# Kernel optimization log

Measured on AMD Instinct MI355X. Metric: run time of the kernel, lower is better.

The kernel has to match this reference:

```python
import jax, jax.numpy as jnp
import numpy as np
import math

B, L, H, E = 4, 2048, 16, 64
S, D = L, E


def setup_inputs() -> dict:
    key = jax.random.key(0)
    kq, kk, kv = jax.random.split(key, 3)
    queries = jax.random.normal(kq, (B, L, H, E), dtype=jnp.float32)
    keys = jax.random.normal(kk, (B, S, H, E), dtype=jnp.float32)
    values = jax.random.normal(kv, (B, S, H, D), dtype=jnp.float32)
    # TriangularCausalMask: True above the diagonal => masked out
    attn_mask = jnp.broadcast_to(
        jnp.triu(jnp.ones((L, S), dtype=bool), k=1)[None, None], (B, 1, L, S)
    )
    return {"queries": queries, "keys": keys, "values": values, "attn_mask": attn_mask}


def reference(queries, keys, values, attn_mask):
    Edim = queries.shape[-1]
    scale = 1.0 / math.sqrt(Edim)  # self.scale is None -> 1/sqrt(E)
    # scores: [B, H, L, S]
    scores = jnp.einsum("blhe,bshe->bhls", queries, keys)
    # mask BEFORE scaling (as in original); -inf is invariant under positive scale
    scores = jnp.where(attn_mask, -jnp.inf, scores)
    attn = jax.nn.softmax(scale * scores, axis=-1)  # dropout p=0.0 -> identity
    out = jnp.einsum("bhls,bshd->blhd", attn, values)
    return out
```

## Files before the change

kernel.cpp:

```cpp
#include <hip/hip_runtime.h>


#define B_ 4
#define L_ 2048
#define H_ 16

typedef __attribute__((ext_vector_type(4))) float f32x4;
typedef __attribute__((ext_vector_type(8))) short bf16x8;

#if __has_builtin(__builtin_amdgcn_exp2f)
#define EXP2(x) __builtin_amdgcn_exp2f(x)
#else
#define EXP2(x) exp2f(x)
#endif

#if __has_builtin(__builtin_amdgcn_sched_barrier)
#define SCHED_FENCE() __builtin_amdgcn_sched_barrier(0)
#else
#define SCHED_FENCE()
#endif

#define BAR() do {                                              \
    SCHED_FENCE();                                              \
    asm volatile("s_waitcnt lgkmcnt(0)" ::: "memory");          \
    __builtin_amdgcn_s_barrier();                               \
    SCHED_FENCE();                                              \
} while (0)

__device__ __forceinline__ unsigned pkbf(float lo, float hi) {
    union { float f; unsigned u; } a, b;
    a.f = lo; b.f = hi;
    return __builtin_amdgcn_perm(b.u, a.u, 0x07060302u);
}

__global__ __launch_bounds__(512, 2) void attn_fwd(
    const float* __restrict__ Q, const float* __restrict__ K,
    const float* __restrict__ V, float* __restrict__ O)
{
    __shared__ unsigned smem[9216];

    const int tid = threadIdx.x;
    const int w   = tid >> 6;
    const int l   = tid & 63;
    const int l15 = l & 15;
    const int qd  = l >> 4;
    const int bh  = blockIdx.x & 63;
    const int g   = blockIdx.x >> 6;
    const int u   = (g < 4) ? g : 11 - g;
    const int b   = bh >> 4, h = bh & 15;
    const float cexp = 0.125f * 1.44269504088896340736f;

    const float* Kb = K + (((size_t)b * L_) * H_ + h) * 64;
    const float* Vb = V + (((size_t)b * L_) * H_ + h) * 64;

    const int t    = 2 * u + (w >> 2);
    const int qr0  = t * 128 + (w & 3) * 32;
    const int mykb = (qr0 >> 6) + 1;
    const int nkb  = 4 * u + 4;

    const int krow = tid >> 3, kq = tid & 7;
    const int kmrow = (((krow >> 2) & 1) << 5) | (((krow >> 5) & 1) << 4)
                    | (((krow >> 3) & 3) << 2) | (krow & 3);
    const int vsp = tid >> 4;
    const int vdg = (tid >> 1) & 7;
    const int vh  = tid & 1;
    const int vswz = vsp ^ (4 * vdg);

    bf16x8 qf[2][2];
#pragma unroll
    for (int rt = 0; rt < 2; ++rt) {
        const int row = qr0 + 16 * rt + l15;
        const float* qp = Q + (((size_t)b * L_ + row) * H_ + h) * 64 + qd * 8;
#pragma unroll
        for (int ke = 0; ke < 2; ++ke) {
            float4 f0 = *(const float4*)(qp + ke * 32);
            float4 f1 = *(const float4*)(qp + ke * 32 + 4);
            union { unsigned u[4]; bf16x8 v; } cv;
            cv.u[0] = pkbf(f0.x * cexp, f0.y * cexp);
            cv.u[1] = pkbf(f0.z * cexp, f0.w * cexp);
            cv.u[2] = pkbf(f1.x * cexp, f1.y * cexp);
            cv.u[3] = pkbf(f1.z * cexp, f1.w * cexp);
            qf[rt][ke] = cv.v;
        }
    }

    f32x4 o[4][2];
#pragma unroll
    for (int dt = 0; dt < 4; ++dt)
#pragma unroll
        for (int rt = 0; rt < 2; ++rt)
            o[dt][rt] = (f32x4){0.f, 0.f, 0.f, 0.f};
    float ls[2] = {0.f, 0.f};

    {
        const float* kg = Kb + (size_t)krow * 1024 + kq * 8;
        float4 k0 = *(const float4*)(kg + 0);
        float4 k1 = *(const float4*)(kg + 4);
        const float* vg = Vb + (size_t)(2 * vsp) * 1024 + vdg * 8 + vh * 4;
        float4 v0 = *(const float4*)(vg + 0);
        float4 v1 = *(const float4*)(vg + 1024);
        unsigned* kd = smem + kmrow * 36 + kq * 4;
        uint4 w0;
        w0.x = pkbf(k0.x, k0.y); w0.y = pkbf(k0.z, k0.w);
        w0.z = pkbf(k1.x, k1.y); w0.w = pkbf(k1.z, k1.w);
        *(uint4*)kd = w0;
        unsigned* vd = smem + 2304 + (8 * vdg + 4 * vh) * 36 + vswz;
        vd[0 * 36] = pkbf(v0.x, v1.x);
        vd[1 * 36] = pkbf(v0.y, v1.y);
        vd[2 * 36] = pkbf(v0.z, v1.z);
        vd[3 * 36] = pkbf(v0.w, v1.w);
    }
    BAR();

    for (int kb = 0; kb < nkb; ++kb) {
        const bool more = (kb + 1 < nkb);
        float4 nk0, nk1, nv0, nv1;
        if (more) {
            const float* kg = Kb + (size_t)((kb + 1) * 64 + krow) * 1024 + kq * 8;
            nk0 = *(const float4*)(kg + 0);
            nk1 = *(const float4*)(kg + 4);
            const float* vg = Vb + (size_t)((kb + 1) * 64 + 2 * vsp) * 1024 + vdg * 8 + vh * 4;
            nv0 = *(const float4*)(vg + 0);
            nv1 = *(const float4*)(vg + 1024);
        }

        if (kb < mykb) {
            const unsigned* Kl = smem + (kb & 1) * 4608;
            const unsigned* Vl = Kl + 2304;

            f32x4 st[4][2];
#pragma unroll
            for (int kt = 0; kt < 4; ++kt)
#pragma unroll
                for (int rt = 0; rt < 2; ++rt)
                    st[kt][rt] = (f32x4){0.f, 0.f, 0.f, 0.f};
#pragma unroll
            for (int kt = 0; kt < 4; ++kt)
#pragma unroll
                for (int ke = 0; ke < 2; ++ke) {
                    bf16x8 a = *(const bf16x8*)(Kl + (kt * 16 + l15) * 36 + ke * 16 + qd * 4);
                    st[kt][0] = __builtin_amdgcn_mfma_f32_16x16x32_bf16(a, qf[0][ke], st[kt][0], 0, 0, 0);
                    st[kt][1] = __builtin_amdgcn_mfma_f32_16x16x32_bf16(a, qf[1][ke], st[kt][1], 0, 0, 0);
                }

            if (kb == mykb - 1) {
#pragma unroll
                for (int kt = 0; kt < 4; ++kt)
#pragma unroll
                    for (int rt = 0; rt < 2; ++rt) {
                        const int rowg = qr0 + 16 * rt + l15;
#pragma unroll
                        for (int r = 0; r < 4; ++r) {
                            const int key = kb * 64 + (kt & 1) * 32 + qd * 8
                                          + (kt >> 1) * 4 + r;
                            if (key > rowg) st[kt][rt][r] = -1e30f;
                        }
                    }
            }

            float sacc0 = 0.f, sacc1 = 0.f;
#pragma unroll
            for (int kt = 0; kt < 4; ++kt)
#pragma unroll
                for (int r = 0; r < 4; ++r) {
                    float p0 = EXP2(st[kt][0][r]);
                    float p1 = EXP2(st[kt][1][r]);
                    st[kt][0][r] = p0;
                    st[kt][1][r] = p1;
                    sacc0 += p0;
                    sacc1 += p1;
                }
            ls[0] += sacc0;
            ls[1] += sacc1;

            bf16x8 vf[2][4];
#pragma unroll
            for (int se = 0; se < 2; ++se)
#pragma unroll
                for (int dt = 0; dt < 4; ++dt) {
                    const int col = (se * 16 + qd * 4) ^ (4 * (2 * dt + (l15 >> 3)));
                    vf[se][dt] = *(const bf16x8*)(Vl + (dt * 16 + l15) * 36 + col);
                }

#pragma unroll
            for (int se = 0; se < 2; ++se)
#pragma unroll
                for (int rt = 0; rt < 2; ++rt) {
                    union { unsigned u[4]; bf16x8 v; } pb;
                    pb.u[0] = pkbf(st[se][rt][0], st[se][rt][1]);
                    pb.u[1] = pkbf(st[se][rt][2], st[se][rt][3]);
                    pb.u[2] = pkbf(st[se + 2][rt][0], st[se + 2][rt][1]);
                    pb.u[3] = pkbf(st[se + 2][rt][2], st[se + 2][rt][3]);
#pragma unroll
                    for (int dt = 0; dt < 4; ++dt)
                        o[dt][rt] = __builtin_amdgcn_mfma_f32_16x16x32_bf16(vf[se][dt], pb.v, o[dt][rt], 0, 0, 0);
                }
        }

        if (more) {
            SCHED_FENCE();
            unsigned* bK = smem + ((kb + 1) & 1) * 4608;
            unsigned* kd = bK + kmrow * 36 + kq * 4;
            uint4 w0;
            w0.x = pkbf(nk0.x, nk0.y); w0.y = pkbf(nk0.z, nk0.w);
            w0.z = pkbf(nk1.x, nk1.y); w0.w = pkbf(nk1.z, nk1.w);
            *(uint4*)kd = w0;
            unsigned* vd = bK + 2304 + (8 * vdg + 4 * vh) * 36 + vswz;
            vd[0 * 36] = pkbf(nv0.x, nv1.x);
            vd[1 * 36] = pkbf(nv0.y, nv1.y);
            vd[2 * 36] = pkbf(nv0.z, nv1.z);
            vd[3 * 36] = pkbf(nv0.w, nv1.w);
            BAR();
        }
    }

#pragma unroll
    for (int rt = 0; rt < 2; ++rt) {
        float s = ls[rt];
        s += __shfl_xor(s, 16);
        s += __shfl_xor(s, 32);
        const float inv = 1.0f / s;
        const int row = qr0 + 16 * rt + l15;
        float* op = O + (((size_t)b * L_ + row) * H_ + h) * 64 + qd * 4;
#pragma unroll
        for (int dt = 0; dt < 4; ++dt) {
            float4 wv;
            wv.x = o[dt][rt][0] * inv;
            wv.y = o[dt][rt][1] * inv;
            wv.z = o[dt][rt][2] * inv;
            wv.w = o[dt][rt][3] * inv;
            *(float4*)(op + dt * 16) = wv;
        }
    }
}

extern "C" void kernel_launch(void* const* d_in, const int* in_sizes, int n_in,
                              void* d_out, int out_size, void* d_ws, size_t ws_size,
                              hipStream_t stream) {
    const float* Q = (const float*)d_in[0];
    const float* K = (const float*)d_in[1];
    const float* V = (const float*)d_in[2];
    float* O = (float*)d_out;

    dim3 grid(64 * 8);
    dim3 block(512);
    hipLaunchKernelGGL(attn_fwd, grid, block, 0, stream, Q, K, V, O);
}
```

Baseline: 199.2 us.

## Process two key blocks per barrier with deeper prefetch and MFMA priority

```diff
diff --git a/kernel.cpp b/kernel.cpp
--- a/kernel.cpp
+++ b/kernel.cpp
@@ -33,11 +33,114 @@
     return __builtin_amdgcn_perm(b.u, a.u, 0x07060302u);
 }
 
-__global__ __launch_bounds__(512, 2) void attn_fwd(
+#define ISSUE1(kbx, S) do {                                                   \
+    const float* kg_ = Kb + (size_t)((kbx) * 64 + krow) * 1024 + kq * 8;      \
+    S##k0 = *(const float4*)(kg_ + 0);                                        \
+    S##k1 = *(const float4*)(kg_ + 4);                                        \
+    const float* vg_ = Vb + (size_t)((kbx) * 64 + 2 * vsp) * 1024             \
+                          + vdg * 8 + vh * 4;                                 \
+    S##v0 = *(const float4*)(vg_ + 0);                                        \
+    S##v1 = *(const float4*)(vg_ + 1024);                                     \
+} while (0)
+
+#define STAGE1(S, hb_) do {                                                   \
+    unsigned* kd_ = (hb_) + kmrow * 36 + kq * 4;                              \
+    uint4 w0_;                                                                \
+    w0_.x = pkbf(S##k0.x, S##k0.y); w0_.y = pkbf(S##k0.z, S##k0.w);           \
+    w0_.z = pkbf(S##k1.x, S##k1.y); w0_.w = pkbf(S##k1.z, S##k1.w);           \
+    *(uint4*)kd_ = w0_;                                                       \
+    unsigned* vd_ = (hb_) + 2304 + (8 * vdg + 4 * vh) * 36 + vswz;            \
+    vd_[0 * 36] = pkbf(S##v0.x, S##v1.x);                                     \
+    vd_[1 * 36] = pkbf(S##v0.y, S##v1.y);                                     \
+    vd_[2 * 36] = pkbf(S##v0.z, S##v1.z);                                     \
+    vd_[3 * 36] = pkbf(S##v0.w, S##v1.w);                                     \
+} while (0)
+
+__device__ __forceinline__ void compute_kb(
+    const unsigned* __restrict__ Kl, int kb, bool diag,
+    const bf16x8 (&qf)[2][2], f32x4 (&o)[4][2], float (&ls)[2],
+    int qr0, int l15, int qd)
+{
+    const unsigned* Vl = Kl + 2304;
+
+    f32x4 st[4][2];
+#pragma unroll
+    for (int kt = 0; kt < 4; ++kt)
+#pragma unroll
+        for (int rt = 0; rt < 2; ++rt)
+            st[kt][rt] = (f32x4){0.f, 0.f, 0.f, 0.f};
+    __builtin_amdgcn_s_setprio(1);
+#pragma unroll
+    for (int kt = 0; kt < 4; ++kt)
+#pragma unroll
+        for (int ke = 0; ke < 2; ++ke) {
+            bf16x8 a = *(const bf16x8*)(Kl + (kt * 16 + l15) * 36 + ke * 16 + qd * 4);
+            st[kt][0] = __builtin_amdgcn_mfma_f32_16x16x32_bf16(a, qf[0][ke], st[kt][0], 0, 0, 0);
+            st[kt][1] = __builtin_amdgcn_mfma_f32_16x16x32_bf16(a, qf[1][ke], st[kt][1], 0, 0, 0);
+        }
+    __builtin_amdgcn_s_setprio(0);
+
+    if (diag) {
+#pragma unroll
+        for (int kt = 0; kt < 4; ++kt)
+#pragma unroll
+            for (int rt = 0; rt < 2; ++rt) {
+                const int rowg = qr0 + 16 * rt + l15;
+#pragma unroll
+                for (int r = 0; r < 4; ++r) {
+                    const int key = kb * 64 + (kt & 1) * 32 + qd * 8
+                                  + (kt >> 1) * 4 + r;
+                    if (key > rowg) st[kt][rt][r] = -1e30f;
+                }
+            }
+    }
+
+    float sacc0 = 0.f, sacc1 = 0.f;
+#pragma unroll
+    for (int kt = 0; kt < 4; ++kt)
+#pragma unroll
+        for (int r = 0; r < 4; ++r) {
+            float p0 = EXP2(st[kt][0][r]);
+            float p1 = EXP2(st[kt][1][r]);
+            st[kt][0][r] = p0;
+            st[kt][1][r] = p1;
+            sacc0 += p0;
+            sacc1 += p1;
+        }
+    ls[0] += sacc0;
+    ls[1] += sacc1;
+
+    bf16x8 vf[2][4];
+#pragma unroll
+    for (int se = 0; se < 2; ++se)
+#pragma unroll
+        for (int dt = 0; dt < 4; ++dt) {
+            const int col = (se * 16 + qd * 4) ^ (4 * (2 * dt + (l15 >> 3)));
+            vf[se][dt] = *(const bf16x8*)(Vl + (dt * 16 + l15) * 36 + col);
+        }
+
+    __builtin_amdgcn_s_setprio(1);
+#pragma unroll
+    for (int se = 0; se < 2; ++se)
+#pragma unroll
+        for (int rt = 0; rt < 2; ++rt) {
+            union { unsigned u[4]; bf16x8 v; } pb;
+            pb.u[0] = pkbf(st[se][rt][0], st[se][rt][1]);
+            pb.u[1] = pkbf(st[se][rt][2], st[se][rt][3]);
+            pb.u[2] = pkbf(st[se + 2][rt][0], st[se + 2][rt][1]);
+            pb.u[3] = pkbf(st[se + 2][rt][2], st[se + 2][rt][3]);
+#pragma unroll
+            for (int dt = 0; dt < 4; ++dt)
+                o[dt][rt] = __builtin_amdgcn_mfma_f32_16x16x32_bf16(vf[se][dt], pb.v, o[dt][rt], 0, 0, 0);
+        }
+    __builtin_amdgcn_s_setprio(0);
+}
+
+__global__ __launch_bounds__(512, 4) void attn_fwd(
     const float* __restrict__ Q, const float* __restrict__ K,
     const float* __restrict__ V, float* __restrict__ O)
 {
-    __shared__ unsigned smem[9216];
+    extern __shared__ unsigned smem[];
 
     const int tid = threadIdx.x;
     const int w   = tid >> 6;
@@ -92,124 +195,35 @@
             o[dt][rt] = (f32x4){0.f, 0.f, 0.f, 0.f};
     float ls[2] = {0.f, 0.f};
 
-    {
-        const float* kg = Kb + (size_t)krow * 1024 + kq * 8;
-        float4 k0 = *(const float4*)(kg + 0);
-        float4 k1 = *(const float4*)(kg + 4);
-        const float* vg = Vb + (size_t)(2 * vsp) * 1024 + vdg * 8 + vh * 4;
-        float4 v0 = *(const float4*)(vg + 0);
-        float4 v1 = *(const float4*)(vg + 1024);
-        unsigned* kd = smem + kmrow * 36 + kq * 4;
-        uint4 w0;
-        w0.x = pkbf(k0.x, k0.y); w0.y = pkbf(k0.z, k0.w);
-        w0.z = pkbf(k1.x, k1.y); w0.w = pkbf(k1.z, k1.w);
-        *(uint4*)kd = w0;
-        unsigned* vd = smem + 2304 + (8 * vdg + 4 * vh) * 36 + vswz;
-        vd[0 * 36] = pkbf(v0.x, v1.x);
-        vd[1 * 36] = pkbf(v0.y, v1.y);
-        vd[2 * 36] = pkbf(v0.z, v1.z);
-        vd[3 * 36] = pkbf(v0.w, v1.w);
-    }
+    float4 Ak0, Ak1, Av0, Av1;
+    float4 Bk0, Bk1, Bv0, Bv1;
+
+    ISSUE1(0, A);
+    ISSUE1(1, B);
+    STAGE1(A, smem);
+    STAGE1(B, smem + 4608);
     BAR();
 
-    for (int kb = 0; kb < nkb; ++kb) {
-        const bool more = (kb + 1 < nkb);
-        float4 nk0, nk1, nv0, nv1;
+    for (int kb2 = 0; kb2 < nkb; kb2 += 2) {
+        unsigned* cur = smem + ((kb2 >> 1) & 1) * 9216;
+        unsigned* nxt = smem + (((kb2 >> 1) & 1) ^ 1) * 9216;
+        const bool more = (kb2 + 2 < nkb);
+
         if (more) {
-            const float* kg = Kb + (size_t)((kb + 1) * 64 + krow) * 1024 + kq * 8;
-            nk0 = *(const float4*)(kg + 0);
-            nk1 = *(const float4*)(kg + 4);
-            const float* vg = Vb + (size_t)((kb + 1) * 64 + 2 * vsp) * 1024 + vdg * 8 + vh * 4;
-            nv0 = *(const float4*)(vg + 0);
-            nv1 = *(const float4*)(vg + 1024);
-        }
-
-        if (kb < mykb) {
-            const unsigned* Kl = smem + (kb & 1) * 4608;
-            const unsigned* Vl = Kl + 2304;
-
-            f32x4 st[4][2];
-#pragma unroll
-            for (int kt = 0; kt < 4; ++kt)
-#pragma unroll
-                for (int rt = 0; rt < 2; ++rt)
-                    st[kt][rt] = (f32x4){0.f, 0.f, 0.f, 0.f};
-#pragma unroll
-            for (int kt = 0; kt < 4; ++kt)
-#pragma unroll
-                for (int ke = 0; ke < 2; ++ke) {
-                    bf16x8 a = *(const bf16x8*)(Kl + (kt * 16 + l15) * 36 + ke * 16 + qd * 4);
-                    st[kt][0] = __builtin_amdgcn_mfma_f32_16x16x32_bf16(a, qf[0][ke], st[kt][0], 0, 0, 0);
-                    st[kt][1] = __builtin_amdgcn_mfma_f32_16x16x32_bf16(a, qf[1][ke], st[kt][1], 0, 0, 0);
-                }
-
-            if (kb == mykb - 1) {
-#pragma unroll
-                for (int kt = 0; kt < 4; ++kt)
-#pragma unroll
-                    for (int rt = 0; rt < 2; ++rt) {
-                        const int rowg = qr0 + 16 * rt + l15;
-#pragma unroll
-                        for (int r = 0; r < 4; ++r) {
-                            const int key = kb * 64 + (kt & 1) * 32 + qd * 8
-                                          + (kt >> 1) * 4 + r;
-                            if (key > rowg) st[kt][rt][r] = -1e30f;
-                        }
-                    }
-            }
-
-            float sacc0 = 0.f, sacc1 = 0.f;
-#pragma unroll
-            for (int kt = 0; kt < 4; ++kt)
-#pragma unroll
-                for (int r = 0; r < 4; ++r) {
-                    float p0 = EXP2(st[kt][0][r]);
-                    float p1 = EXP2(st[kt][1][r]);
-                    st[kt][0][r] = p0;
-                    st[kt][1][r] = p1;
-                    sacc0 += p0;
-                    sacc1 += p1;
-                }
-            ls[0] += sacc0;
-            ls[1] += sacc1;
-
-            bf16x8 vf[2][4];
-#pragma unroll
-            for (int se = 0; se < 2; ++se)
-#pragma unroll
-                for (int dt = 0; dt < 4; ++dt) {
-                    const int col = (se * 16 + qd * 4) ^ (4 * (2 * dt + (l15 >> 3)));
-                    vf[se][dt] = *(const bf16x8*)(Vl + (dt * 16 + l15) * 36 + col);
-                }
-
-#pragma unroll
-            for (int se = 0; se < 2; ++se)
-#pragma unroll
-                for (int rt = 0; rt < 2; ++rt) {
-                    union { unsigned u[4]; bf16x8 v; } pb;
-                    pb.u[0] = pkbf(st[se][rt][0], st[se][rt][1]);
-                    pb.u[1] = pkbf(st[se][rt][2], st[se][rt][3]);
-                    pb.u[2] = pkbf(st[se + 2][rt][0], st[se + 2][rt][1]);
-                    pb.u[3] = pkbf(st[se + 2][rt][2], st[se + 2][rt][3]);
-#pragma unroll
-                    for (int dt = 0; dt < 4; ++dt)
-                        o[dt][rt] = __builtin_amdgcn_mfma_f32_16x16x32_bf16(vf[se][dt], pb.v, o[dt][rt], 0, 0, 0);
-                }
-        }
+            ISSUE1(kb2 + 2, A);
+            ISSUE1(kb2 + 3, B);
+        }
+        SCHED_FENCE();
+
+        if (kb2 < mykb)
+            compute_kb(cur, kb2, kb2 == mykb - 1, qf, o, ls, qr0, l15, qd);
+        if (kb2 + 1 < mykb)
+            compute_kb(cur + 4608, kb2 + 1, kb2 + 1 == mykb - 1, qf, o, ls, qr0, l15, qd);
 
         if (more) {
             SCHED_FENCE();
-            unsigned* bK = smem + ((kb + 1) & 1) * 4608;
-            unsigned* kd = bK + kmrow * 36 + kq * 4;
-            uint4 w0;
-            w0.x = pkbf(nk0.x, nk0.y); w0.y = pkbf(nk0.z, nk0.w);
-            w0.z = pkbf(nk1.x, nk1.y); w0.w = pkbf(nk1.z, nk1.w);
-            *(uint4*)kd = w0;
-            unsigned* vd = bK + 2304 + (8 * vdg + 4 * vh) * 36 + vswz;
-            vd[0 * 36] = pkbf(nv0.x, nv1.x);
-            vd[1 * 36] = pkbf(nv0.y, nv1.y);
-            vd[2 * 36] = pkbf(nv0.z, nv1.z);
-            vd[3 * 36] = pkbf(nv0.w, nv1.w);
+            STAGE1(A, nxt);
+            STAGE1(B, nxt + 4608);
             BAR();
         }
     }
@@ -244,5 +258,5 @@
 
     dim3 grid(64 * 8);
     dim3 block(512);
-    hipLaunchKernelGGL(attn_fwd, grid, block, 0, stream, Q, K, V, O);
-}
+    hipLaunchKernelGGL(attn_fwd, grid, block, 73728, stream, Q, K, V, O);
+}
```

Result: slower. 317.0 us (+59.1%).
